# Kernel optimization log

Hardware: AMD Instinct MI355X
Metric: run time of the kernel (lower is better)

The kernel has to match this reference:

```python
import jax, jax.numpy as jnp
import numpy as np

B, FEAT, H, W = 16, 64, 32, 32


def setup_inputs() -> dict:
    key = jax.random.key(0)
    ks = jax.random.split(key, 8)
    s = 0.05
    return {
        "x": jax.random.normal(ks[0], (B, 2 * FEAT, H, W), jnp.float32),
        # i2s_conv: MaskConv(2F -> 4F, 1x1, maskB with group=1 == all-ones), bias=False
        "w_i2s": jax.random.normal(ks[1], (4 * FEAT, 2 * FEAT), jnp.float32) * s,
        # left/right state-to-state Conv2d(F -> 4F, kernel (2,1)), with bias
        "w_left": jax.random.normal(ks[2], (4 * FEAT, FEAT, 2), jnp.float32) * s,
        "b_left": jax.random.normal(ks[3], (4 * FEAT,), jnp.float32) * s,
        "w_right": jax.random.normal(ks[4], (4 * FEAT, FEAT, 2), jnp.float32) * s,
        "b_right": jax.random.normal(ks[5], (4 * FEAT,), jnp.float32) * s,
        # skip_conv: MaskConv(F -> 2F, 1x1, maskB group=1 == plain conv), bias=True
        "w_skip": jax.random.normal(ks[6], (2 * FEAT, FEAT), jnp.float32) * s,
        "b_skip": jax.random.normal(ks[7], (2 * FEAT,), jnp.float32) * s,
    }


def _shift_right_w(a):  # F.pad(a,(1,0,...))[..., :-1]
    return jnp.pad(a, ((0, 0), (0, 0), (0, 0), (1, 0)))[:, :, :, :-1]


def _shift_left_w(a):  # F.pad(a,(0,1,...))[..., 1:]
    return jnp.pad(a, ((0, 0), (0, 0), (0, 0), (0, 1)))[:, :, :, 1:]


def _shift_down_h(a):  # pad one row on top, drop last row
    return jnp.pad(a, ((0, 0), (0, 0), (1, 0), (0, 0)))[:, :, :-1, :]


def _s2s(hprev, w, b, wshift):
    # pad(top=1, side=1) + Conv2d kernel (2,1) + crop one column, expressed as
    # two 1x1 contractions on width-shifted / (width+height)-shifted maps.
    hw = wshift(hprev)            # [B,F,H,W] shifted one column
    hd = _shift_down_h(hw)        # additionally shifted one row down
    return (jnp.einsum('bchw,oc->bohw', hd, w[:, :, 0])
            + jnp.einsum('bchw,oc->bohw', hw, w[:, :, 1])
            + b[None, :, None, None])


def _forward(x, w_i2s, w_left, b_left, w_right, b_right, w_skip, b_skip):
    b_, c2, h_, w_ = x.shape
    f = c2 // 2
    hmap = jnp.einsum('bchw,oc->bohw', x, w_i2s)  # [B,4F,H,W]
    left_h = hmap   # stew: input-to-state shared between directions
    right_h = hmap
    zeros = jnp.zeros((b_, f, h_, w_), x.dtype)

    def step(carry, _):
        lc, lh, rc, rh = carry
        pre = jax.nn.sigmoid(_s2s(lh, w_left, b_left, _shift_right_w) + left_h)
        o, fg, ig, g = jnp.split(pre, 4, axis=1)
        lc = fg * lc + ig * g
        lh = o * jnp.tanh(lc)
        pre = jax.nn.sigmoid(_s2s(rh, w_right, b_right, _shift_left_w) + right_h)
        o, fg, ig, g = jnp.split(pre, 4, axis=1)
        rc = fg * rc + ig * g
        rh = o * jnp.tanh(rc)
        return (lc, lh, rc, rh), None

    (lc, lh, rc, rh), _ = jax.lax.scan(step, (zeros, zeros, zeros, zeros), None, length=h_)
    rh = _shift_down_h(rh)  # unstew + shift right stream down one row
    out_h = lh + rh         # [B,F,H,W]
    skip = jnp.einsum('bchw,oc->bohw', out_h, w_skip) + b_skip[None, :, None, None]
    return x + skip


def reference(x, w_i2s, w_left, b_left, w_right, b_right, w_skip, b_skip):
    return _forward(x, w_i2s, w_left, b_left, w_right, b_right, w_skip, b_skip)
```

## Files before the change

### kernel.cpp

```cpp
#include <hip/hip_runtime.h>


using bf16   = __bf16;
using bf16x8 = __attribute__((ext_vector_type(8))) __bf16;
using f32x4  = __attribute__((ext_vector_type(4))) float;

#define SCOPE_AGENT __HIP_MEMORY_SCOPE_AGENT

__device__ __forceinline__ float sigf(float x) {
  return __builtin_amdgcn_rcpf(1.0f + __expf(-x));
}
__device__ __forceinline__ float tanh_fast(float x) {
  return 2.0f * __builtin_amdgcn_rcpf(1.0f + __expf(-2.0f * x)) - 1.0f;
}
__device__ __forceinline__ bf16x8 bzero8() {
  bf16x8 v;
#pragma unroll
  for (int e = 0; e < 8; ++e) v[e] = (bf16)0.0f;
  return v;
}
__device__ __forceinline__ unsigned short f2bu(float f) {
  bf16 b = (bf16)f;
  return __builtin_bit_cast(unsigned short, b);
}
__device__ __forceinline__ float bu2f(unsigned short u) {
  return __uint_as_float(((unsigned)u) << 16);
}

__global__ void prep_kernel(const float* __restrict__ w_i2s,
                            const float* __restrict__ w_left,
                            const float* __restrict__ w_right,
                            const float* __restrict__ w_skip,
                            bf16* __restrict__ WnI, bf16* __restrict__ WnL,
                            bf16* __restrict__ WnR, bf16* __restrict__ WnS) {
  int t = blockIdx.x * 256 + threadIdx.x;
  if (t < 32768) {
    WnI[t] = (bf16)w_i2s[t];
    int o = t >> 7, k = t & 127;
    int src = (k < 64) ? (o * 128 + k * 2) : (o * 128 + (k - 64) * 2 + 1);
    WnL[t] = (bf16)w_left[src];
    WnR[t] = (bf16)w_right[src];
    if (t < 8192) WnS[t] = (bf16)w_skip[t];
  }
}

__global__ __launch_bounds__(256, 2)
void hmap_kernel(const float* __restrict__ x, const bf16* __restrict__ Wn,
                 ushort4* __restrict__ hmap2) {
  __shared__ __align__(16) bf16 At[64 * 128];
  const int tile = blockIdx.x;
  const int b = tile >> 4, h0 = (tile & 15) << 1;
  const int t = threadIdx.x;
  const float* xb = x + (size_t)(b * 128) * 1024 + h0 * 32;
#pragma unroll
  for (int i = 0; i < 8; ++i) {
    int idx = t + 256 * i;
    int cc = idx >> 4, m4 = idx & 15;
    f32x4 v = *(const f32x4*)(xb + (size_t)cc * 1024 + m4 * 4);
#pragma unroll
    for (int e = 0; e < 4; ++e) {
      int m = m4 * 4 + e;
      int kb = (cc * 2) ^ ((m & 7) << 4);
      *(bf16*)((char*)At + m * 256 + kb) = (bf16)v[e];
    }
  }
  __syncthreads();
  const int wv = t >> 6, l = t & 63;
  const int l15 = l & 15, lq = l >> 4;
  const int c = wv * 16 + l15;
  bf16x8 bfrag[4][4];
#pragma unroll
  for (int q = 0; q < 4; ++q)
#pragma unroll
    for (int kk = 0; kk < 4; ++kk)
      bfrag[q][kk] = *(const bf16x8*)(Wn + (q * 64 + c) * 128 + kk * 32 + lq * 8);
  f32x4 acc[4][4];
  const f32x4 fz = {0.f, 0.f, 0.f, 0.f};
#pragma unroll
  for (int ms = 0; ms < 4; ++ms)
#pragma unroll
    for (int q = 0; q < 4; ++q) acc[ms][q] = fz;
#pragma unroll
  for (int kk = 0; kk < 4; ++kk) {
#pragma unroll
    for (int ms = 0; ms < 4; ++ms) {
      int m = ms * 16 + l15;
      int kb = ((kk * 32 + lq * 8) * 2) ^ ((m & 7) << 4);
      bf16x8 a = *(const bf16x8*)((const char*)At + m * 256 + kb);
#pragma unroll
      for (int q = 0; q < 4; ++q)
        acc[ms][q] =
            __builtin_amdgcn_mfma_f32_16x16x32_bf16(a, bfrag[q][kk], acc[ms][q], 0, 0, 0);
    }
  }
  const int pix0 = tile * 64;
#pragma unroll
  for (int ms = 0; ms < 4; ++ms)
#pragma unroll
    for (int j = 0; j < 4; ++j) {
      int p = pix0 + ms * 16 + lq * 4 + j;
      ushort4 hv;
      hv.x = f2bu(acc[ms][0][j]);
      hv.y = f2bu(acc[ms][1][j]);
      hv.z = f2bu(acc[ms][2][j]);
      hv.w = f2bu(acc[ms][3][j]);
      hmap2[(size_t)p * 64 + c] = hv;
    }
}

__global__ __launch_bounds__(256, 2)
void scan_kernel(bf16* __restrict__ lhLout, bf16* __restrict__ lhRout,
                 const ushort4* __restrict__ hmap2,
                 const bf16* __restrict__ WnL, const bf16* __restrict__ WnR,
                 const float* __restrict__ bL, const float* __restrict__ bR,
                 bf16* __restrict__ ring, unsigned* __restrict__ prodFlag,
                 unsigned* __restrict__ consFlag) {
  __shared__ __align__(16) bf16 buf[2][3 * 32 * 64];
  const int blk = blockIdx.x;
  const int q = blk & 31, tl = blk >> 5;
  const bool right = (q & 1) != 0;
  const int b = q >> 1;
  const int r0 = tl * 2;
  const int t = threadIdx.x;
  const int dw = right ? 1 : -1;
  bf16* __restrict__ lout = right ? lhRout : lhLout;
  const bf16* __restrict__ Wn = right ? WnR : WnL;
  const float* __restrict__ bias = right ? bR : bL;
  const int wv = t >> 6, l = t & 63, l15 = l & 15, lq = l >> 4;
  const int c = wv * 16 + l15;

#pragma unroll
  for (int i = 0; i < 3; ++i) ((bf16x8*)buf[0])[t + 256 * i] = bzero8();
  ((bf16x8*)buf[1])[t] = bzero8();

  bf16x8 bfrag[4][4];
#pragma unroll
  for (int g = 0; g < 4; ++g)
#pragma unroll
    for (int kk = 0; kk < 4; ++kk)
      bfrag[g][kk] = *(const bf16x8*)(Wn + (g * 64 + c) * 128 + kk * 32 + lq * 8);
  float bq[4];
#pragma unroll
  for (int g = 0; g < 4; ++g) bq[g] = bias[g * 64 + c];
  ushort4 hmp[4][4];
#pragma unroll
  for (int ms = 0; ms < 4; ++ms)
#pragma unroll
    for (int j = 0; j < 4; ++j) {
      int w = (ms & 1) * 16 + lq * 4 + j;
      size_t p = (size_t)((b * 32 + r0 + (ms >> 1)) * 32 + w);
      hmp[ms][j] = hmap2[p * 64 + c];
    }
  float lc_r[4][4];
#pragma unroll
  for (int ms = 0; ms < 4; ++ms)
#pragma unroll
    for (int j = 0; j < 4; ++j) lc_r[ms][j] = 0.0f;

  const unsigned* pBelow = prodFlag + (size_t)(blk - 32) * 32;
  const unsigned* cAbove = consFlag + (size_t)(blk + 32) * 32;
  unsigned* myProd = prodFlag + (size_t)blk * 32;
  unsigned* myCons = consFlag + (size_t)blk * 32;

  __syncthreads();

  for (int s = 0; s < 32; ++s) {
    bf16* curb = buf[s & 1];
    bf16* nxtb = buf[(s + 1) & 1];
    const bool consume = (tl > 0) && (s > 0);
    const bool publish = (tl < 15) && (s < 31);

    if (consume) {
      const unsigned tgt = (unsigned)s;
      while (__hip_atomic_load(pBelow, __ATOMIC_RELAXED, SCOPE_AGENT) < tgt)
        __builtin_amdgcn_s_sleep(1);
      const bf16* slotIn =
          ring + (size_t)((((s - 1) & 7) * 512) + (blk - 32)) * 2048;
      int w = t >> 3, c8 = t & 7;
      const unsigned long long* src =
          (const unsigned long long*)(slotIn + w * 64 + c8 * 8);
      unsigned long long d0 = __hip_atomic_load(src, __ATOMIC_RELAXED, SCOPE_AGENT);
      unsigned long long d1 = __hip_atomic_load(src + 1, __ATOMIC_RELAXED, SCOPE_AGENT);
      int off = (w * 128 + c8 * 16) ^ ((w & 7) << 4);
      *(unsigned long long*)((char*)curb + off) = d0;
      *(unsigned long long*)((char*)curb + off + 8) = d1;
    }
    if (publish && s >= 8) {
      const unsigned tgt = (unsigned)(s - 7);
      while (__hip_atomic_load(cAbove, __ATOMIC_RELAXED, SCOPE_AGENT) < tgt)
        __builtin_amdgcn_s_sleep(1);
    }
    __syncthreads();

    bf16* slotOut = ring + (size_t)(((s & 7) * 512) + blk) * 2048;
#pragma unroll
    for (int ms = 0; ms < 4; ++ms) {
      const int R = 1 + (ms >> 1);
      const int wb_ = (ms & 1) * 16;
      const int wsrc = wb_ + l15 + dw;
      const bool oob = (unsigned)wsrc >= 32u;
      const int wc = wsrc & 31;
      f32x4 acc[4];
      const f32x4 fz = {0.f, 0.f, 0.f, 0.f};
#pragma unroll
      for (int g = 0; g < 4; ++g) acc[g] = fz;
#pragma unroll
      for (int kk = 0; kk < 4; ++kk) {
        const int srcr = (ms >> 1) + (kk >> 1);
        const int c0 = (kk & 1) * 32 + lq * 8;
        int aoff = ((srcr * 32 + wc) * 128 + c0 * 2) ^ ((wc & 7) << 4);
        bf16x8 a = *(const bf16x8*)((const char*)curb + aoff);
        if (oob) a = bzero8();
#pragma unroll
        for (int g = 0; g < 4; ++g)
          acc[g] = __builtin_amdgcn_mfma_f32_16x16x32_bf16(a, bfrag[g][kk], acc[g], 0, 0, 0);
      }
#pragma unroll
      for (int j = 0; j < 4; ++j) {
        const int w = wb_ + lq * 4 + j;
        ushort4 hm = hmp[ms][j];
        float pre0 = acc[0][j] + bu2f(hm.x) + bq[0];
        float pre1 = acc[1][j] + bu2f(hm.y) + bq[1];
        float pre2 = acc[2][j] + bu2f(hm.z) + bq[2];
        float pre3 = acc[3][j] + bu2f(hm.w) + bq[3];
        float og = sigf(pre0), fg = sigf(pre1), ig = sigf(pre2), gg = sigf(pre3);
        float lcv = fg * lc_r[ms][j] + ig * gg;
        lc_r[ms][j] = lcv;
        bf16 vb = (bf16)(og * tanh_fast(lcv));
        int woff = ((R * 32 + w) * 128 + c * 2) ^ ((w & 7) << 4);
        *(bf16*)((char*)nxtb + woff) = vb;
        if (ms >= 2 && publish) {
          unsigned u = (unsigned)__builtin_bit_cast(unsigned short, vb);
          unsigned pv = (unsigned)__shfl_xor((int)u, 1);
          if ((l & 1) == 0) {
            unsigned dword = u | (pv << 16);
            __hip_atomic_store((unsigned*)(slotOut + w * 64 + (c & ~1)), dword,
                               __ATOMIC_RELAXED, SCOPE_AGENT);
          }
        }
      }
    }
    __syncthreads();
    if (publish && t == 0)
      __hip_atomic_store(myProd, (unsigned)(s + 1), __ATOMIC_RELAXED, SCOPE_AGENT);
    if (consume && t == 64)
      __hip_atomic_store(myCons, (unsigned)s, __ATOMIC_RELAXED, SCOPE_AGENT);
  }

#pragma unroll
  for (int i = 0; i < 2; ++i) {
    int idx = t + 256 * i;
    int R = 1 + (idx >> 8), rem = idx & 255;
    int w = rem >> 3, c8 = rem & 7;
    int off = ((R * 32 + w) * 128 + c8 * 16) ^ ((w & 7) << 4);
    bf16x8 v = *(const bf16x8*)((const char*)buf[0] + off);
    *(bf16x8*)(lout + (size_t)((b * 32 + r0 + R - 1) * 32 + w) * 64 + c8 * 8) = v;
  }
}

__global__ __launch_bounds__(256, 2)
void final_kernel(const float* __restrict__ x, const bf16* __restrict__ lhL,
                  const bf16* __restrict__ lhR, const bf16* __restrict__ Wn,
                  const float* __restrict__ b_skip, float* __restrict__ out) {
  __shared__ __align__(16) bf16 At[64 * 64];
  __shared__ __align__(16) float smemT[128 * 72];
  const int tile = blockIdx.x;
  const int b = tile >> 4, h0 = (tile & 15) << 1;
  const int t = threadIdx.x;
#pragma unroll
  for (int i = 0; i < 2; ++i) {
    int idx = t + 256 * i;
    int m = idx >> 3, c8 = idx & 7;
    int h = h0 + (m >> 5), w = m & 31;
    size_t p = (size_t)(b * 32 + h) * 32 + w;
    bf16x8 vL = *(const bf16x8*)(lhL + p * 64 + c8 * 8);
    bf16x8 v;
    if (h > 0) {
      bf16x8 vR = *(const bf16x8*)(lhR + (p - 32) * 64 + c8 * 8);
#pragma unroll
      for (int e = 0; e < 8; ++e) v[e] = (bf16)((float)vL[e] + (float)vR[e]);
    } else {
      v = vL;
    }
    int kb = (c8 * 16) ^ ((m & 7) << 4);
    *(bf16x8*)((char*)At + m * 128 + kb) = v;
  }
  __syncthreads();
  const int wv = t >> 6, l = t & 63;
  const int l15 = l & 15, lq = l >> 4;
  const int c = wv * 16 + l15;
  bf16x8 bfrag[2][2];
#pragma unroll
  for (int g = 0; g < 2; ++g)
#pragma unroll
    for (int kk = 0; kk < 2; ++kk)
      bfrag[g][kk] = *(const bf16x8*)(Wn + (g * 64 + c) * 64 + kk * 32 + lq * 8);
  f32x4 acc[4][2];
  const f32x4 fz = {0.f, 0.f, 0.f, 0.f};
#pragma unroll
  for (int ms = 0; ms < 4; ++ms)
#pragma unroll
    for (int g = 0; g < 2; ++g) acc[ms][g] = fz;
#pragma unroll
  for (int kk = 0; kk < 2; ++kk) {
#pragma unroll
    for (int ms = 0; ms < 4; ++ms) {
      int m = ms * 16 + l15;
      int kb = ((kk * 32 + lq * 8) * 2) ^ ((m & 7) << 4);
      bf16x8 a = *(const bf16x8*)((const char*)At + m * 128 + kb);
#pragma unroll
      for (int g = 0; g < 2; ++g)
        acc[ms][g] =
            __builtin_amdgcn_mfma_f32_16x16x32_bf16(a, bfrag[g][kk], acc[ms][g], 0, 0, 0);
    }
  }
  float bsk[2];
#pragma unroll
  for (int g = 0; g < 2; ++g) bsk[g] = b_skip[g * 64 + c];
#pragma unroll
  for (int ms = 0; ms < 4; ++ms)
#pragma unroll
    for (int g = 0; g < 2; ++g)
#pragma unroll
      for (int j = 0; j < 4; ++j) {
        int m = ms * 16 + lq * 4 + j;
        int n = g * 64 + c;
        smemT[n * 72 + m] = acc[ms][g][j] + bsk[g];
      }
  __syncthreads();
  const float* xb = x + (size_t)(b * 128) * 1024 + h0 * 32;
  float* ob = out + (size_t)(b * 128) * 1024 + h0 * 32;
#pragma unroll
  for (int i = 0; i < 8; ++i) {
    int idx = t + 256 * i;
    int o2 = idx >> 4, m4 = idx & 15;
    f32x4 s = *(const f32x4*)(&smemT[o2 * 72 + m4 * 4]);
    f32x4 xv = *(const f32x4*)(xb + (size_t)o2 * 1024 + m4 * 4);
#pragma unroll
    for (int e = 0; e < 4; ++e) s[e] += xv[e];
    *(f32x4*)(ob + (size_t)o2 * 1024 + m4 * 4) = s;
  }
}

extern "C" void kernel_launch(void* const* d_in, const int* in_sizes, int n_in,
                              void* d_out, int out_size, void* d_ws, size_t ws_size,
                              hipStream_t stream) {
  const float* x       = (const float*)d_in[0];
  const float* w_i2s   = (const float*)d_in[1];
  const float* w_left  = (const float*)d_in[2];
  const float* b_left  = (const float*)d_in[3];
  const float* w_right = (const float*)d_in[4];
  const float* b_right = (const float*)d_in[5];
  const float* w_skip  = (const float*)d_in[6];
  const float* b_skip  = (const float*)d_in[7];
  float* out = (float*)d_out;
  char* ws = (char*)d_ws;

  bf16*     lhL   = (bf16*)(ws + 0x0000000);
  bf16*     lhR   = (bf16*)(ws + 0x0200000);
  ushort4*  hmap2 = (ushort4*)(ws + 0x0400000);
  bf16*     ring  = (bf16*)(ws + 0x0C00000);
  unsigned* prodF = (unsigned*)(ws + 0x1C00000);
  unsigned* consF = (unsigned*)(ws + 0x1C10000);
  bf16*     WnI   = (bf16*)(ws + 0x1C20000);
  bf16*     WnL   = (bf16*)(ws + 0x1C30000);
  bf16*     WnR   = (bf16*)(ws + 0x1C40000);
  bf16*     WnS   = (bf16*)(ws + 0x1C50000);

  hipMemsetAsync(ws + 0x1C00000, 0, 0x20000, stream);
  prep_kernel<<<128, 256, 0, stream>>>(w_i2s, w_left, w_right, w_skip, WnI, WnL, WnR, WnS);
  hmap_kernel<<<256, 256, 0, stream>>>(x, WnI, hmap2);
  scan_kernel<<<512, 256, 0, stream>>>(lhL, lhR, hmap2, WnL, WnR,
                                       b_left, b_right, ring, prodF, consF);
  final_kernel<<<256, 256, 0, stream>>>(x, lhL, lhR, WnS, b_skip, out);
}
```

Measured before the change: 186.5 us.

## Compute boundary rows first to publish early, overlap halo wait; fuse gate reciprocals

Each step now first computes the two output sub-tiles that neighbouring blocks consume, publishes them and raises the producer flag, and only then waits for the halo from the block below and computes the remaining sub-tiles. This shortens the critical path of the inter-block wavefront so the next block can start earlier. The gate maths is also restructured to merge reciprocals (ig*g and o*tanh combined into single rcp calls), cutting transcendental work. The risk is a subtle ordering or race bug in the reordered flag and buffer protocol, plus extra code size.

```diff
diff --git a/kernel.cpp b/kernel.cpp
--- a/kernel.cpp
+++ b/kernel.cpp
@@ -7,12 +7,6 @@
 
 #define SCOPE_AGENT __HIP_MEMORY_SCOPE_AGENT
 
-__device__ __forceinline__ float sigf(float x) {
-  return __builtin_amdgcn_rcpf(1.0f + __expf(-x));
-}
-__device__ __forceinline__ float tanh_fast(float x) {
-  return 2.0f * __builtin_amdgcn_rcpf(1.0f + __expf(-2.0f * x)) - 1.0f;
-}
 __device__ __forceinline__ bf16x8 bzero8() {
   bf16x8 v;
 #pragma unroll
@@ -25,6 +19,12 @@
 }
 __device__ __forceinline__ float bu2f(unsigned short u) {
   return __uint_as_float(((unsigned)u) << 16);
+}
+__device__ __forceinline__ float sigf(float x) {
+  return __builtin_amdgcn_rcpf(1.0f + __expf(-x));
+}
+__device__ __forceinline__ float tanh_fast(float x) {
+  return 2.0f * __builtin_amdgcn_rcpf(1.0f + __expf(-2.0f * x)) - 1.0f;
 }
 
 __global__ void prep_kernel(const float* __restrict__ w_i2s,
@@ -169,6 +169,66 @@
     bf16* nxtb = buf[(s + 1) & 1];
     const bool consume = (tl > 0) && (s > 0);
     const bool publish = (tl < 15) && (s < 31);
+    bf16* slotOut = ring + (size_t)(((s & 7) * 512) + blk) * 2048;
+
+    if (publish && s >= 8) {
+      const unsigned tgt = (unsigned)(s - 7);
+      while (__hip_atomic_load(cAbove, __ATOMIC_RELAXED, SCOPE_AGENT) < tgt)
+        __builtin_amdgcn_s_sleep(1);
+    }
+
+#pragma unroll
+    for (int ms = 2; ms < 4; ++ms) {
+      const int wb_ = (ms & 1) * 16;
+      const int wsrc = wb_ + l15 + dw;
+      const bool oob = (unsigned)wsrc >= 32u;
+      const int wc = wsrc & 31;
+      f32x4 acc[4];
+      const f32x4 fz = {0.f, 0.f, 0.f, 0.f};
+#pragma unroll
+      for (int g = 0; g < 4; ++g) acc[g] = fz;
+#pragma unroll
+      for (int kk = 0; kk < 4; ++kk) {
+        const int srcr = 1 + (kk >> 1);
+        const int c0 = (kk & 1) * 32 + lq * 8;
+        int aoff = ((srcr * 32 + wc) * 128 + c0 * 2) ^ ((wc & 7) << 4);
+        bf16x8 a = *(const bf16x8*)((const char*)curb + aoff);
+        if (oob) a = bzero8();
+#pragma unroll
+        for (int g = 0; g < 4; ++g)
+          acc[g] = __builtin_amdgcn_mfma_f32_16x16x32_bf16(a, bfrag[g][kk], acc[g], 0, 0, 0);
+      }
+#pragma unroll
+      for (int j = 0; j < 4; ++j) {
+        const int w = wb_ + lq * 4 + j;
+        ushort4 hm = hmp[ms][j];
+        float e0 = __expf(-(acc[0][j] + bu2f(hm.x) + bq[0]));
+        float e1 = __expf(-(acc[1][j] + bu2f(hm.y) + bq[1]));
+        float e2 = __expf(-(acc[2][j] + bu2f(hm.z) + bq[2]));
+        float e3 = __expf(-(acc[3][j] + bu2f(hm.w) + bq[3]));
+        float fg = __builtin_amdgcn_rcpf(1.0f + e1);
+        float igg = __builtin_amdgcn_rcpf((1.0f + e2) * (1.0f + e3));
+        float lcv = fg * lc_r[ms][j] + igg;
+        lc_r[ms][j] = lcv;
+        float ey = __expf(-2.0f * lcv);
+        float lh = (1.0f - ey) * __builtin_amdgcn_rcpf((1.0f + e0) * (1.0f + ey));
+        bf16 vb = (bf16)lh;
+        int woff = ((2 * 32 + w) * 128 + c * 2) ^ ((w & 7) << 4);
+        *(bf16*)((char*)nxtb + woff) = vb;
+        if (publish) {
+          unsigned u = (unsigned)__builtin_bit_cast(unsigned short, vb);
+          unsigned pv = (unsigned)__shfl_xor((int)u, 1);
+          if ((l & 1) == 0) {
+            unsigned dword = u | (pv << 16);
+            __hip_atomic_store((unsigned*)(slotOut + w * 64 + (c & ~1)), dword,
+                               __ATOMIC_RELAXED, SCOPE_AGENT);
+          }
+        }
+      }
+    }
+    __syncthreads();
+    if (publish && t == 0)
+      __hip_atomic_store(myProd, (unsigned)(s + 1), __ATOMIC_RELAXED, SCOPE_AGENT);
 
     if (consume) {
       const unsigned tgt = (unsigned)s;
@@ -185,17 +245,12 @@
       *(unsigned long long*)((char*)curb + off) = d0;
       *(unsigned long long*)((char*)curb + off + 8) = d1;
     }
-    if (publish && s >= 8) {
-      const unsigned tgt = (unsigned)(s - 7);
-      while (__hip_atomic_load(cAbove, __ATOMIC_RELAXED, SCOPE_AGENT) < tgt)
-        __builtin_amdgcn_s_sleep(1);
-    }
     __syncthreads();
-
-    bf16* slotOut = ring + (size_t)(((s & 7) * 512) + blk) * 2048;
-#pragma unroll
-    for (int ms = 0; ms < 4; ++ms) {
-      const int R = 1 + (ms >> 1);
+    if (consume && t == 0)
+      __hip_atomic_store(myCons, (unsigned)s, __ATOMIC_RELAXED, SCOPE_AGENT);
+
+#pragma unroll
+    for (int ms = 0; ms < 2; ++ms) {
       const int wb_ = (ms & 1) * 16;
       const int wsrc = wb_ + l15 + dw;
       const bool oob = (unsigned)wsrc >= 32u;
@@ -206,7 +261,7 @@
       for (int g = 0; g < 4; ++g) acc[g] = fz;
 #pragma unroll
       for (int kk = 0; kk < 4; ++kk) {
-        const int srcr = (ms >> 1) + (kk >> 1);
+        const int srcr = kk >> 1;
         const int c0 = (kk & 1) * 32 + lq * 8;
         int aoff = ((srcr * 32 + wc) * 128 + c0 * 2) ^ ((wc & 7) << 4);
         bf16x8 a = *(const bf16x8*)((const char*)curb + aoff);
@@ -219,32 +274,21 @@
       for (int j = 0; j < 4; ++j) {
         const int w = wb_ + lq * 4 + j;
         ushort4 hm = hmp[ms][j];
-        float pre0 = acc[0][j] + bu2f(hm.x) + bq[0];
-        float pre1 = acc[1][j] + bu2f(hm.y) + bq[1];
-        float pre2 = acc[2][j] + bu2f(hm.z) + bq[2];
-        float pre3 = acc[3][j] + bu2f(hm.w) + bq[3];
-        float og = sigf(pre0), fg = sigf(pre1), ig = sigf(pre2), gg = sigf(pre3);
-        float lcv = fg * lc_r[ms][j] + ig * gg;
+        float e0 = __expf(-(acc[0][j] + bu2f(hm.x) + bq[0]));
+        float e1 = __expf(-(acc[1][j] + bu2f(hm.y) + bq[1]));
+        float e2 = __expf(-(acc[2][j] + bu2f(hm.z) + bq[2]));
+        float e3 = __expf(-(acc[3][j] + bu2f(hm.w) + bq[3]));
+        float fg = __builtin_amdgcn_rcpf(1.0f + e1);
+        float igg = __builtin_amdgcn_rcpf((1.0f + e2) * (1.0f + e3));
+        float lcv = fg * lc_r[ms][j] + igg;
         lc_r[ms][j] = lcv;
-        bf16 vb = (bf16)(og * tanh_fast(lcv));
-        int woff = ((R * 32 + w) * 128 + c * 2) ^ ((w & 7) << 4);
-        *(bf16*)((char*)nxtb + woff) = vb;
-        if (ms >= 2 && publish) {
-          unsigned u = (unsigned)__builtin_bit_cast(unsigned short, vb);
-          unsigned pv = (unsigned)__shfl_xor((int)u, 1);
-          if ((l & 1) == 0) {
-            unsigned dword = u | (pv << 16);
-            __hip_atomic_store((unsigned*)(slotOut + w * 64 + (c & ~1)), dword,
-                               __ATOMIC_RELAXED, SCOPE_AGENT);
-          }
-        }
+        float ey = __expf(-2.0f * lcv);
+        float lh = (1.0f - ey) * __builtin_amdgcn_rcpf((1.0f + e0) * (1.0f + ey));
+        int woff = ((1 * 32 + w) * 128 + c * 2) ^ ((w & 7) << 4);
+        *(bf16*)((char*)nxtb + woff) = (bf16)lh;
       }
     }
     __syncthreads();
-    if (publish && t == 0)
-      __hip_atomic_store(myProd, (unsigned)(s + 1), __ATOMIC_RELAXED, SCOPE_AGENT);
-    if (consume && t == 64)
-      __hip_atomic_store(myCons, (unsigned)s, __ATOMIC_RELAXED, SCOPE_AGENT);
   }
 
 #pragma unroll
```

New measurement: 176.8 us. 5.2% less time.
